# Kernel tuning notes

Hardware: AMD Instinct MI355X
Metric: run time of the kernel (lower is better)

The kernel has to match this reference:

```python
import jax, jax.numpy as jnp
import numpy as np

BN_EPS = 1e-5


def maxpool2(x):
    # 2x2 max pool, stride 2: (B,C,H,W) -> (B,C,H//2,W//2)
    B, C, H, W = x.shape
    return x.reshape(B, C, H // 2, 2, W // 2, 2).max(axis=(3, 5))


def setup_inputs() -> dict:
    key = jax.random.key(0)
    ks = jax.random.split(key, 6)
    B, C, H, W = 4, 64, 96, 96   # in_dim = 64
    K, OD = 64, 64               # key_dim, out_dim
    sc = lambda fan: 1.0 / np.sqrt(fan)
    return {
        "c2": jax.random.normal(ks[0], (B, C, H, W), jnp.float32),
        "x": jax.random.normal(ks[1], (B, C, H, W), jnp.float32),
        # edge_att: Conv2d(2C->OD, 1x1, no bias) -> BN -> ReLU -> Conv2d(OD->1, 1x1) -> Sigmoid
        "w_ea1": jax.random.normal(ks[2], (OD, 2 * C), jnp.float32) * sc(2 * C),
        "bn_w": jnp.ones((OD,), jnp.float32),
        "bn_b": jnp.zeros((OD,), jnp.float32),
        "bn_m": jnp.zeros((OD,), jnp.float32),
        "bn_v": jnp.ones((OD,), jnp.float32),
        "w_ea2": jax.random.normal(ks[3], (1, OD), jnp.float32) * sc(OD),
        "b_ea2": jnp.zeros((1,), jnp.float32),
        # query_conv (shared for query AND key in the original forward)
        "w_q": jax.random.normal(ks[4], (K, C), jnp.float32) * sc(C),
        "b_q": jnp.zeros((K,), jnp.float32),
        "gamma": jnp.full((1,), 0.5, jnp.float32),
    }


def reference(c2, x, w_ea1, bn_w, bn_b, bn_m, bn_v, w_ea2, b_ea2, w_q, b_q, gamma):
    xp = maxpool2(x)        # (B,C,Hp,Wp)
    c2p = maxpool2(c2)
    B, C, H, W = x.shape
    Hp, Wp = xp.shape[2], xp.shape[3]

    # edge attention gate on pooled features -> (B,1,Hp,Wp)
    cat = jnp.concatenate([c2p, xp], axis=1)                       # (B,2C,Hp,Wp)
    h = jnp.einsum('oc,bchw->bohw', w_ea1, cat)
    bn_scale = (bn_w / jnp.sqrt(bn_v + BN_EPS))[None, :, None, None]
    h = jax.nn.relu((h - bn_m[None, :, None, None]) * bn_scale + bn_b[None, :, None, None])
    ea = jax.nn.sigmoid(jnp.einsum('oc,bchw->bohw', w_ea2, h) + b_ea2[None, :, None, None])

    # query at full res, key at pooled res (SAME conv weights, as in the source)
    q = jnp.einsum('kc,bchw->bkhw', w_q, x) + b_q[None, :, None, None]    # (B,K,H,W)
    k = jnp.einsum('kc,bchw->bkhw', w_q, xp) + b_q[None, :, None, None]   # (B,K,Hp,Wp)

    pq = q.reshape(B, -1, H * W)        # (B,K,N)
    pk = k.reshape(B, -1, Hp * Wp)      # (B,K,M)
    energy = jnp.einsum('bkn,bkm->bnm', pq, pk)                    # (B,N,M)
    attn = jax.nn.softmax(energy * ea.reshape(B, 1, Hp * Wp), axis=-1)

    v = xp.reshape(B, C, Hp * Wp)                                   # (B,C,M)
    out = jnp.einsum('bcm,bnm->bcn', v, attn).reshape(B, C, H, W)
    return gamma[0] * out + x
```

## Files before the change

### kernel.cpp

```cpp
#include <hip/hip_runtime.h>
#include <stdint.h>

#define B_ 4
#define C_ 64
#define H_ 96
#define W_ 96
#define HP_ 48
#define WP_ 48
#define N_ (H_*W_)
#define M_ (HP_*WP_)
#define KD_ 64
#define OD_ 64
#define BN_EPS 1e-5f
#define LOG2E 1.4426950408889634f
#define SHIFT2 28.853900817779268f
#define QT_ 48
#define QI_ (QT_/16)
#define QB_ (N_/QT_)
#define NT_ (M_/64)

typedef __bf16 bf16_t;
typedef bf16_t bf16x8 __attribute__((ext_vector_type(8)));
typedef bf16_t bf16x4 __attribute__((ext_vector_type(4)));
typedef float f32x4 __attribute__((ext_vector_type(4)));
typedef short short4v __attribute__((ext_vector_type(4)));

static __device__ __forceinline__ unsigned short f2bf(float f) {
    unsigned int u = __builtin_bit_cast(unsigned int, f);
    u += 0x7fffu + ((u >> 16) & 1u);
    return (unsigned short)(u >> 16);
}

static __device__ __forceinline__ f32x4 mfma16_bf16(short4v a, short4v b, f32x4 c) {
#if __has_builtin(__builtin_amdgcn_mfma_f32_16x16x16bf16_1k)
    return __builtin_amdgcn_mfma_f32_16x16x16bf16_1k(a, b, c, 0, 0, 0);
#else
    return c;
#endif
}

static __device__ __forceinline__ void gl_lds16(const unsigned short* g, unsigned short* l) {
#if __has_builtin(__builtin_amdgcn_global_load_lds)
    __builtin_amdgcn_global_load_lds(
        (const __attribute__((address_space(1))) unsigned int*)(const void*)g,
        (__attribute__((address_space(3))) unsigned int*)(void*)l, 16, 0, 0);
#endif
}

static __device__ __forceinline__ void setprio1() {
#if __has_builtin(__builtin_amdgcn_s_setprio)
    __builtin_amdgcn_s_setprio(1);
#endif
}
static __device__ __forceinline__ void setprio0() {
#if __has_builtin(__builtin_amdgcn_s_setprio)
    __builtin_amdgcn_s_setprio(0);
#endif
}
static __device__ __forceinline__ void schedbar0() {
#if __has_builtin(__builtin_amdgcn_sched_barrier)
    __builtin_amdgcn_sched_barrier(0);
#endif
}
static __device__ __forceinline__ void rawbar() {
#if __has_builtin(__builtin_amdgcn_s_barrier)
    __builtin_amdgcn_s_barrier();
#else
    __syncthreads();
#endif
}

__global__ __launch_bounds__(256) void prep_kernel(
    const float* __restrict__ x, const float* __restrict__ c2,
    const float* __restrict__ wq, const float* __restrict__ bq,
    const float* __restrict__ w1, const float* __restrict__ bnw, const float* __restrict__ bnb,
    const float* __restrict__ bnm, const float* __restrict__ bnv,
    const float* __restrict__ w2, const float* __restrict__ b2,
    unsigned short* __restrict__ kb, unsigned short* __restrict__ vb, float* __restrict__ ea) {

    __shared__ float lw1[OD_*2*C_];
    __shared__ float lwq[KD_*C_];
    __shared__ float xs[C_*33];
    __shared__ float c2s[C_*33];
    __shared__ float red[8][32];

    int tid = threadIdx.x;
    int b = blockIdx.x / 72;
    int m0 = (blockIdx.x % 72) * 32;

    for (int i = tid; i < OD_*2*C_; i += 256) lw1[i] = w1[i];
    for (int i = tid; i < KD_*C_; i += 256) lwq[i] = wq[i];
    for (int j = tid; j < 2048; j += 256) {
        int c = j >> 5, p = j & 31;
        int m = m0 + p;
        int hp = m / WP_, wp = m % WP_;
        size_t base = ((size_t)(b*C_ + c)*H_ + 2*hp)*W_ + 2*wp;
        const float* px = x + base;
        float mx = fmaxf(fmaxf(px[0], px[1]), fmaxf(px[W_], px[W_+1]));
        xs[c*33 + p] = mx;
        vb[(size_t)(b*C_ + c)*M_ + m] = f2bf(mx);
        const float* pc = c2 + base;
        c2s[c*33 + p] = fmaxf(fmaxf(pc[0], pc[1]), fmaxf(pc[W_], pc[W_+1]));
    }
    __syncthreads();

    int ml = tid & 31, oz = tid >> 5;
    int m = m0 + ml;

    float h[8] = {0,0,0,0,0,0,0,0};
    for (int c = 0; c < C_; c += 4) {
        float x0 = xs[c*33+ml], x1 = xs[(c+1)*33+ml], x2 = xs[(c+2)*33+ml], x3 = xs[(c+3)*33+ml];
        #pragma unroll
        for (int oi = 0; oi < 8; oi++) {
            const float4 wv = *(const float4*)&lwq[(oz*8 + oi)*C_ + c];
            h[oi] = fmaf(wv.x, x0, fmaf(wv.y, x1, fmaf(wv.z, x2, fmaf(wv.w, x3, h[oi]))));
        }
    }
    unsigned short tmp[8];
    #pragma unroll
    for (int oi = 0; oi < 8; oi++) tmp[oi] = f2bf(h[oi] + bq[oz*8 + oi]);
    *(uint4*)&kb[((size_t)b*M_ + m)*KD_ + oz*8] = *(const uint4*)tmp;

    float g[8] = {0,0,0,0,0,0,0,0};
    for (int c = 0; c < 2*C_; c += 4) {
        const float* srcb = (c < C_) ? &c2s[c*33] : &xs[(c - C_)*33];
        float x0 = srcb[ml], x1 = srcb[33+ml], x2 = srcb[66+ml], x3 = srcb[99+ml];
        #pragma unroll
        for (int oi = 0; oi < 8; oi++) {
            const float4 wv = *(const float4*)&lw1[(oz*8 + oi)*(2*C_) + c];
            g[oi] = fmaf(wv.x, x0, fmaf(wv.y, x1, fmaf(wv.z, x2, fmaf(wv.w, x3, g[oi]))));
        }
    }
    float z = 0.f;
    #pragma unroll
    for (int oi = 0; oi < 8; oi++) {
        int o = oz*8 + oi;
        float sc = bnw[o] * rsqrtf(bnv[o] + BN_EPS);
        float t = (g[oi] - bnm[o]) * sc + bnb[o];
        z += w2[o] * fmaxf(t, 0.f);
    }
    red[oz][ml] = z;
    __syncthreads();
    if (oz == 0) {
        float s = b2[0];
        #pragma unroll
        for (int i = 0; i < 8; i++) s += red[i][ml];
        ea[(size_t)b*M_ + m] = LOG2E / (1.f + __builtin_amdgcn_exp2f(-s * LOG2E));
    }
}

__global__ __launch_bounds__(256, 3) void attn_kernel(
    const float* __restrict__ wq, const float* __restrict__ bq,
    const unsigned short* __restrict__ kb, const unsigned short* __restrict__ vb,
    const float* __restrict__ ea, const float* __restrict__ x,
    const float* __restrict__ gamma_p, float* __restrict__ out) {

    __shared__ __align__(16) char smem[41984];

    int tid = threadIdx.x;
    int wave = tid >> 6, lane = tid & 63, quad = lane >> 4, l16 = lane & 15;
    int blk = blockIdx.x;
    int b = (blk & 7) >> 1;
    int n_base = ((blk & 1) * (QB_/2) + (blk >> 3)) * QT_;
    int xsw = l16 & 7;

    unsigned short* qlds = (unsigned short*)(smem + 32768);
    {
        const float* xb = x + (size_t)b*C_*N_ + n_base;
        bf16x8 wh0, wh1, wl0, wl1;
        {
            float w8[8];
            unsigned short hs[8], ls[8];
            const float* wp0 = wq + (size_t)(wave*16 + l16)*C_ + quad*8;
            *(float4*)&w8[0] = *(const float4*)wp0;
            *(float4*)&w8[4] = *(const float4*)(wp0 + 4);
            #pragma unroll
            for (int j = 0; j < 8; j++) {
                hs[j] = f2bf(w8[j]);
                float hf = __builtin_bit_cast(float, (unsigned int)hs[j] << 16);
                ls[j] = f2bf(w8[j] - hf);
            }
            wh0 = __builtin_bit_cast(bf16x8, *(const uint4*)hs);
            wl0 = __builtin_bit_cast(bf16x8, *(const uint4*)ls);
            const float* wp1 = wp0 + 32;
            *(float4*)&w8[0] = *(const float4*)wp1;
            *(float4*)&w8[4] = *(const float4*)(wp1 + 4);
            #pragma unroll
            for (int j = 0; j < 8; j++) {
                hs[j] = f2bf(w8[j]);
                float hf = __builtin_bit_cast(float, (unsigned int)hs[j] << 16);
                ls[j] = f2bf(w8[j] - hf);
            }
            wh1 = __builtin_bit_cast(bf16x8, *(const uint4*)hs);
            wl1 = __builtin_bit_cast(bf16x8, *(const uint4*)ls);
        }
        float4 bq4 = *(const float4*)(bq + wave*16 + quad*4);

        f32x4 qacc[3];
        #pragma unroll
        for (int t = 0; t < 3; t++) qacc[t] = (f32x4){0.f,0.f,0.f,0.f};

        #pragma unroll
        for (int t = 0; t < 3; t++) {
            #pragma unroll
            for (int h = 0; h < 2; h++) {
                float v8[8];
                #pragma unroll
                for (int j = 0; j < 8; j++)
                    v8[j] = xb[(size_t)(h*32 + quad*8 + j)*N_ + t*16 + l16];
                unsigned short hs[8], ls[8];
                #pragma unroll
                for (int j = 0; j < 8; j++) {
                    hs[j] = f2bf(v8[j]);
                    float hf = __builtin_bit_cast(float, (unsigned int)hs[j] << 16);
                    ls[j] = f2bf(v8[j] - hf);
                }
                bf16x8 xh = __builtin_bit_cast(bf16x8, *(const uint4*)hs);
                bf16x8 xl = __builtin_bit_cast(bf16x8, *(const uint4*)ls);
                bf16x8 wh = h ? wh1 : wh0;
                bf16x8 wl = h ? wl1 : wl0;
#if __has_builtin(__builtin_amdgcn_mfma_f32_16x16x32_bf16)
                qacc[t] = __builtin_amdgcn_mfma_f32_16x16x32_bf16(wh, xh, qacc[t], 0, 0, 0);
                qacc[t] = __builtin_amdgcn_mfma_f32_16x16x32_bf16(wl, xh, qacc[t], 0, 0, 0);
                qacc[t] = __builtin_amdgcn_mfma_f32_16x16x32_bf16(wh, xl, qacc[t], 0, 0, 0);
#endif
            }
        }
        #pragma unroll
        for (int t = 0; t < 3; t++) {
            unsigned short q4[4];
            q4[0] = f2bf(qacc[t][0] + bq4.x);
            q4[1] = f2bf(qacc[t][1] + bq4.y);
            q4[2] = f2bf(qacc[t][2] + bq4.z);
            q4[3] = f2bf(qacc[t][3] + bq4.w);
            int n_abs = t*16 + l16;
            int kc = wave*2 + (quad >> 1);
            *(uint2*)&qlds[n_abs*64 + ((kc ^ (n_abs & 7)) << 3) + (quad & 1)*4] =
                *(const uint2*)q4;
        }
    }
    asm volatile("s_waitcnt lgkmcnt(0)" ::: "memory");
    __syncthreads();

    bf16x8 qf[QI_][2];
    #pragma unroll
    for (int qi = 0; qi < QI_; qi++) {
        const unsigned short* qp = qlds + (qi*16 + l16)*64;
        qf[qi][0] = __builtin_bit_cast(bf16x8, *(const uint4*)(qp + ((quad     ^ xsw) << 3)));
        qf[qi][1] = __builtin_bit_cast(bf16x8, *(const uint4*)(qp + (((quad+4) ^ xsw) << 3)));
    }
    asm volatile("s_waitcnt lgkmcnt(0)" ::: "memory");
    __syncthreads();

    f32x4 o2[QI_][4];
    f32x4 lacc[QI_];
    #pragma unroll
    for (int qi = 0; qi < QI_; qi++) {
        lacc[qi] = (f32x4){0.f,0.f,0.f,0.f};
        #pragma unroll
        for (int ct = 0; ct < 4; ct++) o2[qi][ct] = (f32x4){0.f,0.f,0.f,0.f};
    }
    const short one_bf = (short)0x3F80;
    short4v ones = (short4v){one_bf, one_bf, one_bf, one_bf};

    const unsigned short* kbB = kb + (size_t)b*M_*KD_;
    const unsigned short* vbB = vb + (size_t)b*C_*M_;
    const float* eaB = ea + (size_t)b*M_;

    int srow = tid >> 3;
    int ksw  = ((tid & 7) ^ (srow & 7)) << 3;

    auto STAGE = [&](int mb, char* kd, char* vd) {
        unsigned short* kds = (unsigned short*)kd;
        unsigned short* vds = (unsigned short*)vd;
        gl_lds16(kbB + (size_t)(mb + srow)*KD_      + ksw, kds + tid*8);
        gl_lds16(kbB + (size_t)(mb + srow + 32)*KD_ + ksw, kds + 2048 + tid*8);
        gl_lds16(vbB + (size_t)srow*M_      + mb + ksw, vds + tid*8);
        gl_lds16(vbB + (size_t)(srow+32)*M_ + mb + ksw, vds + 2048 + tid*8);
    };

    {
        const f32x4* eaV = (const f32x4*)eaB;
        f32x4* eaL = (f32x4*)(smem + 32768);
        for (int i = tid; i < M_/4; i += 256) eaL[i] = eaV[i];
    }
    asm volatile("s_waitcnt lgkmcnt(0)" ::: "memory");
    __syncthreads();
    STAGE(0,  smem,          smem + 8192);
    STAGE(64, smem + 16384,  smem + 16384 + 8192);
    asm volatile("s_waitcnt vmcnt(4)" ::: "memory");
    rawbar();
    asm volatile("" ::: "memory");

    const float* lds_ea = (const float*)(smem + 32768);
    int krow = wave*16 + l16;

    struct FragSet { bf16x8 kf0, kf1; short4v va0, va1, va2, va3; f32x4 e4; };
    FragSet fA, fB;

    {
        unsigned short* kc = (unsigned short*)smem;
        unsigned short* vc = (unsigned short*)(smem + 8192);
        fA.e4  = *(const f32x4*)&lds_ea[0*64 + wave*16 + quad*4];
        fA.kf0 = __builtin_bit_cast(bf16x8, *(const uint4*)(kc + krow*KD_ + (((quad  ) ^ xsw) << 3)));
        fA.kf1 = __builtin_bit_cast(bf16x8, *(const uint4*)(kc + krow*KD_ + (((quad+4) ^ xsw) << 3)));
        fA.va0 = *(const short4v*)(vc + (0*16 + l16)*64 + (((wave*2 + (quad>>1)) ^ xsw) << 3) + (quad&1)*4);
        fA.va1 = *(const short4v*)(vc + (1*16 + l16)*64 + (((wave*2 + (quad>>1)) ^ xsw) << 3) + (quad&1)*4);
        fA.va2 = *(const short4v*)(vc + (2*16 + l16)*64 + (((wave*2 + (quad>>1)) ^ xsw) << 3) + (quad&1)*4);
        fA.va3 = *(const short4v*)(vc + (3*16 + l16)*64 + (((wave*2 + (quad>>1)) ^ xsw) << 3) + (quad&1)*4);
    }

#define ATTN_STEP(T_, CUR, NXT)                                                        \
    {                                                                                  \
        const int t_ = (T_);                                                           \
        if (t_ < NT_ - 1) {                                                            \
            asm volatile("s_waitcnt vmcnt(0)" ::: "memory");   \
            schedbar0();                                                               \
            rawbar();                                \
            asm volatile("" ::: "memory");                                             \
            schedbar0();                                                               \
            if (t_ + 2 < NT_) {                                                        \
                char* nb = smem + (t_ & 1) * 16384;                                    \
                STAGE((t_ + 2) * 64, nb, nb + 8192);                                   \
            }                                                                          \
            unsigned short* kc_ = (unsigned short*)(smem + ((t_ + 1) & 1) * 16384);    \
            unsigned short* vc_ = (unsigned short*)(smem + ((t_ + 1) & 1) * 16384 + 8192); \
            NXT.e4  = *(const f32x4*)&lds_ea[(t_ + 1)*64 + wave*16 + quad*4];          \
            NXT.kf0 = __builtin_bit_cast(bf16x8, *(const uint4*)(kc_ + krow*KD_ + (((quad  ) ^ xsw) << 3))); \
            NXT.kf1 = __builtin_bit_cast(bf16x8, *(const uint4*)(kc_ + krow*KD_ + (((quad+4) ^ xsw) << 3))); \
            NXT.va0 = *(const short4v*)(vc_ + (0*16 + l16)*64 + (((wave*2 + (quad>>1)) ^ xsw) << 3) + (quad&1)*4); \
            NXT.va1 = *(const short4v*)(vc_ + (1*16 + l16)*64 + (((wave*2 + (quad>>1)) ^ xsw) << 3) + (quad&1)*4); \
            NXT.va2 = *(const short4v*)(vc_ + (2*16 + l16)*64 + (((wave*2 + (quad>>1)) ^ xsw) << 3) + (quad&1)*4); \
            NXT.va3 = *(const short4v*)(vc_ + (3*16 + l16)*64 + (((wave*2 + (quad>>1)) ^ xsw) << 3) + (quad&1)*4); \
            schedbar0();                                                               \
            asm volatile("s_waitcnt lgkmcnt(7)" ::: "memory");   \
            schedbar0();                                                               \
        } else {                                                                       \
            schedbar0();                                                               \
            asm volatile("s_waitcnt lgkmcnt(0)" ::: "memory");      \
            schedbar0();                                                               \
        }                                                                              \
                               \
        f32x4 st[QI_];                                                                 \
        setprio1();                                                                    \
        _Pragma("unroll")                                                              \
        for (int qi = 0; qi < QI_; qi++) {                                             \
            f32x4 z = (f32x4){0.f,0.f,0.f,0.f};                                        \
            z = __builtin_amdgcn_mfma_f32_16x16x32_bf16(CUR.kf0, qf[qi][0], z, 0, 0, 0); \
            z = __builtin_amdgcn_mfma_f32_16x16x32_bf16(CUR.kf1, qf[qi][1], z, 0, 0, 0); \
            st[qi] = z;                                                                \
        }                                                                              \
        setprio0();                                                                    \
        short4v pk[QI_];                                                               \
        _Pragma("unroll")                                                              \
        for (int qi = 0; qi < QI_; qi++) {                                             \
            f32x4 p;                                                                   \
            p[0] = __builtin_amdgcn_exp2f(fmaf(st[qi][0], CUR.e4[0], -SHIFT2));        \
            p[1] = __builtin_amdgcn_exp2f(fmaf(st[qi][1], CUR.e4[1], -SHIFT2));        \
            p[2] = __builtin_amdgcn_exp2f(fmaf(st[qi][2], CUR.e4[2], -SHIFT2));        \
            p[3] = __builtin_amdgcn_exp2f(fmaf(st[qi][3], CUR.e4[3], -SHIFT2));        \
            pk[qi] = __builtin_bit_cast(short4v, __builtin_convertvector(p, bf16x4));  \
        }                                                                              \
        setprio1();                                                                    \
        _Pragma("unroll")                                                              \
        for (int qi = 0; qi < QI_; qi++) {                                             \
            o2[qi][0] = mfma16_bf16(CUR.va0, pk[qi], o2[qi][0]);                       \
            o2[qi][1] = mfma16_bf16(CUR.va1, pk[qi], o2[qi][1]);                       \
            o2[qi][2] = mfma16_bf16(CUR.va2, pk[qi], o2[qi][2]);                       \
            o2[qi][3] = mfma16_bf16(CUR.va3, pk[qi], o2[qi][3]);                       \
            lacc[qi]  = mfma16_bf16(ones,    pk[qi], lacc[qi]);                        \
        }                                                                              \
        setprio0();                                                                    \
    }

    for (int t = 0; t < NT_; t += 2) {
        ATTN_STEP(t,     fA, fB);
        ATTN_STEP(t + 1, fB, fA);
    }
#undef ATTN_STEP

    __syncthreads();

    float* o_red0 = (float*)smem;
    float* o_red1 = o_red0 + QT_*68;
    float* l_red  = o_red1 + QT_*68;

    if (lane < 16) {
        #pragma unroll
        for (int qi = 0; qi < QI_; qi++) l_red[wave*QT_ + qi*16 + l16] = lacc[qi][0];
    }
    if (wave < 2) {
        float* od = (wave == 0) ? o_red0 : o_red1;
        #pragma unroll
        for (int qi = 0; qi < QI_; qi++)
            #pragma unroll
            for (int ct = 0; ct < 4; ct++)
                *(f32x4*)&od[(qi*16 + l16)*68 + ct*16 + quad*4] = o2[qi][ct];
    }
    __syncthreads();
    if (wave >= 2) {
        float* od = (wave == 2) ? o_red0 : o_red1;
        #pragma unroll
        for (int qi = 0; qi < QI_; qi++)
            #pragma unroll
            for (int ct = 0; ct < 4; ct++) {
                f32x4* p = (f32x4*)&od[(qi*16 + l16)*68 + ct*16 + quad*4];
                *p += o2[qi][ct];
            }
    }
    __syncthreads();
    if (tid < QT_) {
        float s = (l_red[tid] + l_red[QT_ + tid]) + (l_red[2*QT_ + tid] + l_red[3*QT_ + tid]);
        l_red[tid] = 1.f / s;
    }
    __syncthreads();

    float gmm = gamma_p[0];
    int c = tid >> 2, q4 = tid & 3;
    const float* xrow = x + ((size_t)b*C_ + c)*N_ + n_base;
    float* orow = out + ((size_t)b*C_ + c)*N_ + n_base;
    #pragma unroll
    for (int i = 0; i < QI_; i++) {
        int q0 = q4*4 + i*16;
        float4 xv = *(const float4*)(xrow + q0);
        float4 ov;
        float v0 = (o_red0[(q0+0)*68 + c] + o_red1[(q0+0)*68 + c]) * l_red[q0+0];
        float v1 = (o_red0[(q0+1)*68 + c] + o_red1[(q0+1)*68 + c]) * l_red[q0+1];
        float v2 = (o_red0[(q0+2)*68 + c] + o_red1[(q0+2)*68 + c]) * l_red[q0+2];
        float v3 = (o_red0[(q0+3)*68 + c] + o_red1[(q0+3)*68 + c]) * l_red[q0+3];
        ov.x = fmaf(gmm, v0, xv.x);
        ov.y = fmaf(gmm, v1, xv.y);
        ov.z = fmaf(gmm, v2, xv.z);
        ov.w = fmaf(gmm, v3, xv.w);
        *(float4*)(orow + q0) = ov;
    }
}

extern "C" void kernel_launch(void* const* d_in, const int* in_sizes, int n_in,
                              void* d_out, int out_size, void* d_ws, size_t ws_size,
                              hipStream_t stream) {
    const float* c2    = (const float*)d_in[0];
    const float* x     = (const float*)d_in[1];
    const float* w_ea1 = (const float*)d_in[2];
    const float* bn_w  = (const float*)d_in[3];
    const float* bn_b  = (const float*)d_in[4];
    const float* bn_m  = (const float*)d_in[5];
    const float* bn_v  = (const float*)d_in[6];
    const float* w_ea2 = (const float*)d_in[7];
    const float* b_ea2 = (const float*)d_in[8];
    const float* w_q   = (const float*)d_in[9];
    const float* b_q   = (const float*)d_in[10];
    const float* gamma = (const float*)d_in[11];
    float* out = (float*)d_out;

    char* ws = (char*)d_ws;
    float* ea            = (float*)(ws + 0);
    unsigned short* kb   = (unsigned short*)(ws + 36864);
    unsigned short* vb   = (unsigned short*)(ws + 1216512);

    prep_kernel<<<dim3((B_*M_)/32), dim3(256), 0, stream>>>(x, c2, w_q, b_q,
        w_ea1, bn_w, bn_b, bn_m, bn_v, w_ea2, b_ea2, kb, vb, ea);
    attn_kernel<<<dim3(B_*QB_), dim3(256), 0, stream>>>(w_q, b_q, kb, vb, ea, x, gamma, out);
}
```

Baseline: 148.0 us.

## Double KV tile to 128 and use 16x16x32 MFMA for PV product

Doubles the key/value block per pipeline step from 64 to 128, halving the number of barrier/wait iterations, and permutes the K row layout so each lane's two score fragments concatenate into an 8-wide bf16 operand. This lets the PV and row-sum products use the 16x16x32 bf16 MFMA instead of 16x16x16, halving those instruction counts. LDS usage grows to about 73KB and occupancy drops from 3 to 2 blocks per CU, with more registers held per fragment set, which risks lower latency hiding.

After: 148.0 us. About the same (-0.0%).

```diff
diff --git a/kernel.cpp b/kernel.cpp
--- a/kernel.cpp
+++ b/kernel.cpp
@@ -17,26 +17,23 @@
 #define QT_ 48
 #define QI_ (QT_/16)
 #define QB_ (N_/QT_)
-#define NT_ (M_/64)
+#define KVB_ 128
+#define NT2_ (M_/KVB_)
+#define KBUF_ 16384
+#define BUF_ 32768
+#define EAOFF_ 65536
 
 typedef __bf16 bf16_t;
 typedef bf16_t bf16x8 __attribute__((ext_vector_type(8)));
 typedef bf16_t bf16x4 __attribute__((ext_vector_type(4)));
 typedef float f32x4 __attribute__((ext_vector_type(4)));
 typedef short short4v __attribute__((ext_vector_type(4)));
+typedef short short8v __attribute__((ext_vector_type(8)));
 
 static __device__ __forceinline__ unsigned short f2bf(float f) {
     unsigned int u = __builtin_bit_cast(unsigned int, f);
     u += 0x7fffu + ((u >> 16) & 1u);
     return (unsigned short)(u >> 16);
-}
-
-static __device__ __forceinline__ f32x4 mfma16_bf16(short4v a, short4v b, f32x4 c) {
-#if __has_builtin(__builtin_amdgcn_mfma_f32_16x16x16bf16_1k)
-    return __builtin_amdgcn_mfma_f32_16x16x16bf16_1k(a, b, c, 0, 0, 0);
-#else
-    return c;
-#endif
 }
 
 static __device__ __forceinline__ void gl_lds16(const unsigned short* g, unsigned short* l) {
@@ -149,13 +146,13 @@
     }
 }
 
-__global__ __launch_bounds__(256, 3) void attn_kernel(
+__global__ __launch_bounds__(256, 2) void attn_kernel(
     const float* __restrict__ wq, const float* __restrict__ bq,
     const unsigned short* __restrict__ kb, const unsigned short* __restrict__ vb,
     const float* __restrict__ ea, const float* __restrict__ x,
     const float* __restrict__ gamma_p, float* __restrict__ out) {
 
-    __shared__ __align__(16) char smem[41984];
+    __shared__ __align__(16) char smem[74752];
 
     int tid = threadIdx.x;
     int wave = tid >> 6, lane = tid & 63, quad = lane >> 4, l16 = lane & 15;
@@ -164,7 +161,7 @@
     int n_base = ((blk & 1) * (QB_/2) + (blk >> 3)) * QT_;
     int xsw = l16 & 7;
 
-    unsigned short* qlds = (unsigned short*)(smem + 32768);
+    unsigned short* qlds = (unsigned short*)(smem + EAOFF_);
     {
         const float* xb = x + (size_t)b*C_*N_ + n_base;
         bf16x8 wh0, wh1, wl0, wl1;
@@ -260,80 +257,100 @@
         #pragma unroll
         for (int ct = 0; ct < 4; ct++) o2[qi][ct] = (f32x4){0.f,0.f,0.f,0.f};
     }
-    const short one_bf = (short)0x3F80;
-    short4v ones = (short4v){one_bf, one_bf, one_bf, one_bf};
+    const unsigned short ones_u[8] = {0x3F80,0x3F80,0x3F80,0x3F80,0x3F80,0x3F80,0x3F80,0x3F80};
+    bf16x8 ones8 = __builtin_bit_cast(bf16x8, *(const uint4*)ones_u);
 
     const unsigned short* kbB = kb + (size_t)b*M_*KD_;
     const unsigned short* vbB = vb + (size_t)b*C_*M_;
     const float* eaB = ea + (size_t)b*M_;
 
-    int srow = tid >> 3;
-    int ksw  = ((tid & 7) ^ (srow & 7)) << 3;
-
-    auto STAGE = [&](int mb, char* kd, char* vd) {
-        unsigned short* kds = (unsigned short*)kd;
-        unsigned short* vds = (unsigned short*)vd;
-        gl_lds16(kbB + (size_t)(mb + srow)*KD_      + ksw, kds + tid*8);
-        gl_lds16(kbB + (size_t)(mb + srow + 32)*KD_ + ksw, kds + 2048 + tid*8);
-        gl_lds16(vbB + (size_t)srow*M_      + mb + ksw, vds + tid*8);
-        gl_lds16(vbB + (size_t)(srow+32)*M_ + mb + ksw, vds + 2048 + tid*8);
+    int r8  = tid >> 3;
+    int mloc = (((r8 & 15) >> 2) << 3) + ((r8 >> 4) << 2) + (r8 & 3);
+    int kcs = ((tid & 7) ^ (r8 & 7)) << 3;
+    int c16 = tid >> 4;
+    int vcs = ((tid & 15) ^ (c16 & 7)) << 3;
+
+    auto STAGE = [&](int mb, char* buf) {
+        unsigned short* kd = (unsigned short*)buf;
+        unsigned short* vd = (unsigned short*)(buf + KBUF_);
+        gl_lds16(kbB + (size_t)(mb +  0 + mloc)*KD_ + kcs, kd + 0*2048 + tid*8);
+        gl_lds16(kbB + (size_t)(mb + 32 + mloc)*KD_ + kcs, kd + 1*2048 + tid*8);
+        gl_lds16(kbB + (size_t)(mb + 64 + mloc)*KD_ + kcs, kd + 2*2048 + tid*8);
+        gl_lds16(kbB + (size_t)(mb + 96 + mloc)*KD_ + kcs, kd + 3*2048 + tid*8);
+        gl_lds16(vbB + (size_t)( 0 + c16)*M_ + mb + vcs, vd + 0*2048 + tid*8);
+        gl_lds16(vbB + (size_t)(16 + c16)*M_ + mb + vcs, vd + 1*2048 + tid*8);
+        gl_lds16(vbB + (size_t)(32 + c16)*M_ + mb + vcs, vd + 2*2048 + tid*8);
+        gl_lds16(vbB + (size_t)(48 + c16)*M_ + mb + vcs, vd + 3*2048 + tid*8);
     };
 
     {
         const f32x4* eaV = (const f32x4*)eaB;
-        f32x4* eaL = (f32x4*)(smem + 32768);
+        f32x4* eaL = (f32x4*)(smem + EAOFF_);
         for (int i = tid; i < M_/4; i += 256) eaL[i] = eaV[i];
     }
     asm volatile("s_waitcnt lgkmcnt(0)" ::: "memory");
     __syncthreads();
-    STAGE(0,  smem,          smem + 8192);
-    STAGE(64, smem + 16384,  smem + 16384 + 8192);
-    asm volatile("s_waitcnt vmcnt(4)" ::: "memory");
+    STAGE(0,    smem);
+    STAGE(128,  smem + BUF_);
+    asm volatile("s_waitcnt vmcnt(8)" ::: "memory");
     rawbar();
     asm volatile("" ::: "memory");
 
-    const float* lds_ea = (const float*)(smem + 32768);
-    int krow = wave*16 + l16;
-
-    struct FragSet { bf16x8 kf0, kf1; short4v va0, va1, va2, va3; f32x4 e4; };
+    const float* lds_ea = (const float*)(smem + EAOFF_);
+
+    int kOffA0 = (wave*32 + l16)*64 + ((quad       ^ xsw) << 3);
+    int kOffA1 = (wave*32 + l16)*64 + (((quad + 4) ^ xsw) << 3);
+    int kOffB0 = kOffA0 + 16*64;
+    int kOffB1 = kOffA1 + 16*64;
+    int vch    = ((wave*4 + quad) ^ xsw) << 3;
+    int eaIdx  = wave*32 + quad*8;
+
+    struct FragSet {
+        bf16x8 kfA0, kfA1, kfB0, kfB1;
+        bf16x8 va0, va1, va2, va3;
+        f32x4 eA, eB;
+    };
     FragSet fA, fB;
 
     {
         unsigned short* kc = (unsigned short*)smem;
-        unsigned short* vc = (unsigned short*)(smem + 8192);
-        fA.e4  = *(const f32x4*)&lds_ea[0*64 + wave*16 + quad*4];
-        fA.kf0 = __builtin_bit_cast(bf16x8, *(const uint4*)(kc + krow*KD_ + (((quad  ) ^ xsw) << 3)));
-        fA.kf1 = __builtin_bit_cast(bf16x8, *(const uint4*)(kc + krow*KD_ + (((quad+4) ^ xsw) << 3)));
-        fA.va0 = *(const short4v*)(vc + (0*16 + l16)*64 + (((wave*2 + (quad>>1)) ^ xsw) << 3) + (quad&1)*4);
-        fA.va1 = *(const short4v*)(vc + (1*16 + l16)*64 + (((wave*2 + (quad>>1)) ^ xsw) << 3) + (quad&1)*4);
-        fA.va2 = *(const short4v*)(vc + (2*16 + l16)*64 + (((wave*2 + (quad>>1)) ^ xsw) << 3) + (quad&1)*4);
-        fA.va3 = *(const short4v*)(vc + (3*16 + l16)*64 + (((wave*2 + (quad>>1)) ^ xsw) << 3) + (quad&1)*4);
+        unsigned short* vc = (unsigned short*)(smem + KBUF_);
+        fA.eA  = *(const f32x4*)&lds_ea[0*KVB_ + eaIdx];
+        fA.eB  = *(const f32x4*)&lds_ea[0*KVB_ + eaIdx + 4];
+        fA.kfA0 = __builtin_bit_cast(bf16x8, *(const uint4*)(kc + kOffA0));
+        fA.kfA1 = __builtin_bit_cast(bf16x8, *(const uint4*)(kc + kOffA1));
+        fA.kfB0 = __builtin_bit_cast(bf16x8, *(const uint4*)(kc + kOffB0));
+        fA.kfB1 = __builtin_bit_cast(bf16x8, *(const uint4*)(kc + kOffB1));
+        fA.va0 = __builtin_bit_cast(bf16x8, *(const uint4*)(vc + (0*16 + l16)*KVB_ + vch));
+        fA.va1 = __builtin_bit_cast(bf16x8, *(const uint4*)(vc + (1*16 + l16)*KVB_ + vch));
+        fA.va2 = __builtin_bit_cast(bf16x8, *(const uint4*)(vc + (2*16 + l16)*KVB_ + vch));
+        fA.va3 = __builtin_bit_cast(bf16x8, *(const uint4*)(vc + (3*16 + l16)*KVB_ + vch));
     }
 
 #define ATTN_STEP(T_, CUR, NXT)                                                        \
     {                                                                                  \
         const int t_ = (T_);                                                           \
-        if (t_ < NT_ - 1) {                                                            \
+        if (t_ < NT2_ - 1) {                                                           \
             asm volatile("s_waitcnt vmcnt(0)" ::: "memory");   \
             schedbar0();                                                               \
-            rawbar();                                \
+            rawbar();                    \
             asm volatile("" ::: "memory");                                             \
             schedbar0();                                                               \
-            if (t_ + 2 < NT_) {                                                        \
-                char* nb = smem + (t_ & 1) * 16384;                                    \
-                STAGE((t_ + 2) * 64, nb, nb + 8192);                                   \
-            }                                                                          \
-            unsigned short* kc_ = (unsigned short*)(smem + ((t_ + 1) & 1) * 16384);    \
-            unsigned short* vc_ = (unsigned short*)(smem + ((t_ + 1) & 1) * 16384 + 8192); \
-            NXT.e4  = *(const f32x4*)&lds_ea[(t_ + 1)*64 + wave*16 + quad*4];          \
-            NXT.kf0 = __builtin_bit_cast(bf16x8, *(const uint4*)(kc_ + krow*KD_ + (((quad  ) ^ xsw) << 3))); \
-            NXT.kf1 = __builtin_bit_cast(bf16x8, *(const uint4*)(kc_ + krow*KD_ + (((quad+4) ^ xsw) << 3))); \
-            NXT.va0 = *(const short4v*)(vc_ + (0*16 + l16)*64 + (((wave*2 + (quad>>1)) ^ xsw) << 3) + (quad&1)*4); \
-            NXT.va1 = *(const short4v*)(vc_ + (1*16 + l16)*64 + (((wave*2 + (quad>>1)) ^ xsw) << 3) + (quad&1)*4); \
-            NXT.va2 = *(const short4v*)(vc_ + (2*16 + l16)*64 + (((wave*2 + (quad>>1)) ^ xsw) << 3) + (quad&1)*4); \
-            NXT.va3 = *(const short4v*)(vc_ + (3*16 + l16)*64 + (((wave*2 + (quad>>1)) ^ xsw) << 3) + (quad&1)*4); \
-            schedbar0();                                                               \
-            asm volatile("s_waitcnt lgkmcnt(7)" ::: "memory");   \
+            if (t_ + 2 < NT2_) { STAGE((t_ + 2)*KVB_, smem + (t_ & 1)*BUF_); }         \
+            unsigned short* kc_ = (unsigned short*)(smem + ((t_ + 1) & 1)*BUF_);       \
+            unsigned short* vc_ = (unsigned short*)(smem + ((t_ + 1) & 1)*BUF_ + KBUF_); \
+            NXT.eA  = *(const f32x4*)&lds_ea[(t_ + 1)*KVB_ + eaIdx];                   \
+            NXT.eB  = *(const f32x4*)&lds_ea[(t_ + 1)*KVB_ + eaIdx + 4];               \
+            NXT.kfA0 = __builtin_bit_cast(bf16x8, *(const uint4*)(kc_ + kOffA0));      \
+            NXT.kfA1 = __builtin_bit_cast(bf16x8, *(const uint4*)(kc_ + kOffA1));      \
+            NXT.kfB0 = __builtin_bit_cast(bf16x8, *(const uint4*)(kc_ + kOffB0));      \
+            NXT.kfB1 = __builtin_bit_cast(bf16x8, *(const uint4*)(kc_ + kOffB1));      \
+            NXT.va0 = __builtin_bit_cast(bf16x8, *(const uint4*)(vc_ + (0*16 + l16)*KVB_ + vch)); \
+            NXT.va1 = __builtin_bit_cast(bf16x8, *(const uint4*)(vc_ + (1*16 + l16)*KVB_ + vch)); \
+            NXT.va2 = __builtin_bit_cast(bf16x8, *(const uint4*)(vc_ + (2*16 + l16)*KVB_ + vch)); \
+            NXT.va3 = __builtin_bit_cast(bf16x8, *(const uint4*)(vc_ + (3*16 + l16)*KVB_ + vch)); \
+            schedbar0();                                                               \
+            asm volatile("s_waitcnt lgkmcnt(10)" ::: "memory");  \
             schedbar0();                                                               \
         } else {                                                                       \
             schedbar0();                                                               \
@@ -341,39 +358,50 @@
             schedbar0();                                                               \
         }                                                                              \
                                \
-        f32x4 st[QI_];                                                                 \
+        f32x4 stA[QI_], stB[QI_];                                                      \
         setprio1();                                                                    \
         _Pragma("unroll")                                                              \
         for (int qi = 0; qi < QI_; qi++) {                                             \
-            f32x4 z = (f32x4){0.f,0.f,0.f,0.f};                                        \
-            z = __builtin_amdgcn_mfma_f32_16x16x32_bf16(CUR.kf0, qf[qi][0], z, 0, 0, 0); \
-            z = __builtin_amdgcn_mfma_f32_16x16x32_bf16(CUR.kf1, qf[qi][1], z, 0, 0, 0); \
-            st[qi] = z;                                                                \
+            f32x4 zA = (f32x4){0.f,0.f,0.f,0.f};                                       \
+            zA = __builtin_amdgcn_mfma_f32_16x16x32_bf16(CUR.kfA0, qf[qi][0], zA, 0, 0, 0); \
+            zA = __builtin_amdgcn_mfma_f32_16x16x32_bf16(CUR.kfA1, qf[qi][1], zA, 0, 0, 0); \
+            stA[qi] = zA;                                                              \
+            f32x4 zB = (f32x4){0.f,0.f,0.f,0.f};                                       \
+            zB = __builtin_amdgcn_mfma_f32_16x16x32_bf16(CUR.kfB0, qf[qi][0], zB, 0, 0, 0); \
+            zB = __builtin_amdgcn_mfma_f32_16x16x32_bf16(CUR.kfB1, qf[qi][1], zB, 0, 0, 0); \
+            stB[qi] = zB;                                                              \
         }                                                                              \
         setprio0();                                                                    \
-        short4v pk[QI_];                                                               \
+        bf16x8 pk[QI_];                                                                \
         _Pragma("unroll")                                                              \
         for (int qi = 0; qi < QI_; qi++) {                                             \
-            f32x4 p;                                                                   \
-            p[0] = __builtin_amdgcn_exp2f(fmaf(st[qi][0], CUR.e4[0], -SHIFT2));        \
-            p[1] = __builtin_amdgcn_exp2f(fmaf(st[qi][1], CUR.e4[1], -SHIFT2));        \
-            p[2] = __builtin_amdgcn_exp2f(fmaf(st[qi][2], CUR.e4[2], -SHIFT2));        \
-            p[3] = __builtin_amdgcn_exp2f(fmaf(st[qi][3], CUR.e4[3], -SHIFT2));        \
-            pk[qi] = __builtin_bit_cast(short4v, __builtin_convertvector(p, bf16x4));  \
+            f32x4 pA, pB;                                                              \
+            pA[0] = __builtin_amdgcn_exp2f(fmaf(stA[qi][0], CUR.eA[0], -SHIFT2));      \
+            pA[1] = __builtin_amdgcn_exp2f(fmaf(stA[qi][1], CUR.eA[1], -SHIFT2));      \
+            pA[2] = __builtin_amdgcn_exp2f(fmaf(stA[qi][2], CUR.eA[2], -SHIFT2));      \
+            pA[3] = __builtin_amdgcn_exp2f(fmaf(stA[qi][3], CUR.eA[3], -SHIFT2));      \
+            pB[0] = __builtin_amdgcn_exp2f(fmaf(stB[qi][0], CUR.eB[0], -SHIFT2));      \
+            pB[1] = __builtin_amdgcn_exp2f(fmaf(stB[qi][1], CUR.eB[1], -SHIFT2));      \
+            pB[2] = __builtin_amdgcn_exp2f(fmaf(stB[qi][2], CUR.eB[2], -SHIFT2));      \
+            pB[3] = __builtin_amdgcn_exp2f(fmaf(stB[qi][3], CUR.eB[3], -SHIFT2));      \
+            short4v pa = __builtin_bit_cast(short4v, __builtin_convertvector(pA, bf16x4)); \
+            short4v pb = __builtin_bit_cast(short4v, __builtin_convertvector(pB, bf16x4)); \
+            short8v p8 = __builtin_shufflevector(pa, pb, 0, 1, 2, 3, 4, 5, 6, 7);      \
+            pk[qi] = __builtin_bit_cast(bf16x8, p8);                                   \
         }                                                                              \
         setprio1();                                                                    \
         _Pragma("unroll")                                                              \
         for (int qi = 0; qi < QI_; qi++) {                                             \
-            o2[qi][0] = mfma16_bf16(CUR.va0, pk[qi], o2[qi][0]);                       \
-            o2[qi][1] = mfma16_bf16(CUR.va1, pk[qi], o2[qi][1]);                       \
-            o2[qi][2] = mfma16_bf16(CUR.va2, pk[qi], o2[qi][2]);                       \
-            o2[qi][3] = mfma16_bf16(CUR.va3, pk[qi], o2[qi][3]);                       \
-            lacc[qi]  = mfma16_bf16(ones,    pk[qi], lacc[qi]);                        \
+            o2[qi][0] = __builtin_amdgcn_mfma_f32_16x16x32_bf16(CUR.va0, pk[qi], o2[qi][0], 0, 0, 0); \
+            o2[qi][1] = __builtin_amdgcn_mfma_f32_16x16x32_bf16(CUR.va1, pk[qi], o2[qi][1], 0, 0, 0); \
+            o2[qi][2] = __builtin_amdgcn_mfma_f32_16x16x32_bf16(CUR.va2, pk[qi], o2[qi][2], 0, 0, 0); \
+            o2[qi][3] = __builtin_amdgcn_mfma_f32_16x16x32_bf16(CUR.va3, pk[qi], o2[qi][3], 0, 0, 0); \
+            lacc[qi]  = __builtin_amdgcn_mfma_f32_16x16x32_bf16(ones8,   pk[qi], lacc[qi], 0, 0, 0); \
         }                                                                              \
         setprio0();                                                                    \
     }
 
-    for (int t = 0; t < NT_; t += 2) {
+    for (int t = 0; t < NT2_; t += 2) {
         ATTN_STEP(t,     fA, fB);
         ATTN_STEP(t + 1, fB, fA);
     }
```
